# Kernel optimization log

Measured on AMD Instinct MI355X. Metric: run time of the kernel, lower is better.

## Reference

```python
import jax, jax.numpy as jnp
import numpy as np

N_NODES = 50000
N_EDGES = 800000
D_IN = 128
HIDDEN = [128, 128]
D_OUT = 64


def setup_inputs() -> dict:
    key = jax.random.key(0)
    ks = jax.random.split(key, 12)
    x = jax.random.normal(ks[0], (N_NODES, D_IN), dtype=jnp.float32)
    edge_index = jax.random.randint(ks[1], (2, N_EDGES), 0, N_NODES, dtype=jnp.int64)
    # SAGEConv params: lin_l acts on aggregated neighbors (has bias), lin_r on root
    def lin(k, fan_in, fan_out):
        s = 1.0 / np.sqrt(fan_in)
        return jax.random.uniform(k, (fan_in, fan_out), jnp.float32, -s, s)
    dims = [D_IN] + HIDDEN
    inp = {"x": x, "edge_index": edge_index}
    for i in range(len(HIDDEN)):
        inp[f"Wl{i}"] = lin(ks[2 + 3 * i], dims[i], dims[i + 1])
        inp[f"Wr{i}"] = lin(ks[3 + 3 * i], dims[i], dims[i + 1])
        inp[f"b{i}"] = jnp.zeros((dims[i + 1],), jnp.float32)
    inp["Wfc"] = lin(ks[10], HIDDEN[-1], D_OUT)
    inp["bfc"] = jnp.zeros((D_OUT,), jnp.float32)
    return inp


def _sage_conv(x, src, dst, n, Wl, Wr, b, deg_inv):
    # mean-aggregate source features into destination nodes
    agg = jax.ops.segment_sum(x[src], dst, num_segments=n) * deg_inv[:, None]
    return agg @ Wl + x @ Wr + b


def reference(x, edge_index, Wl0, Wr0, b0, Wl1, Wr1, b1, Wfc, bfc):
    src, dst = edge_index[0], edge_index[1]
    n = x.shape[0]
    deg = jax.ops.segment_sum(jnp.ones((src.shape[0],), x.dtype), dst, num_segments=n)
    deg_inv = 1.0 / jnp.maximum(deg, 1.0)
    h = jax.nn.relu(_sage_conv(x, src, dst, n, Wl0, Wr0, b0, deg_inv))
    # dropout p=0 / eval mode -> identity
    h = jax.nn.relu(_sage_conv(h, src, dst, n, Wl1, Wr1, b1, deg_inv))
    return h @ Wfc + bfc
```

## Files before the change

### kernel.cpp

```cpp
#include <hip/hip_runtime.h>
#include <hip/hip_bf16.h>

#define NN 50000
#define NE 800000
#define D 128
#define DOUT 64
#define PAD 64
#define BSH 8
#define NBUCK 196
#define CHUNK 4096
#define NBINB 196
#define SEGC 56
#define N8 (NN * D / 8)

typedef __attribute__((ext_vector_type(8))) short short8;
typedef __attribute__((ext_vector_type(4))) float float4v;


__device__ inline unsigned short f2bf(float f) {
    union { float f; unsigned int i; } c; c.f = f;
    unsigned int u = c.i;
    return (unsigned short)((u + 0x7fffu + ((u >> 16) & 1u)) >> 16);
}
__device__ inline float bflo(unsigned int u) {
    union { unsigned int i; float f; } c; c.i = u << 16; return c.f;
}
__device__ inline float bfhi(unsigned int u) {
    union { unsigned int i; float f; } c; c.i = u & 0xffff0000u; return c.f;
}


struct Stage1Args {
    const int* src;
    const int* dst;
    unsigned int* binned;
    int* cnts;
    const float* W[5];
    unsigned short* P[5];
    const float* x;
    unsigned short* xb;
    unsigned short* zrow;
};

__global__ void stage1(Stage1Args args) {
    int blk = blockIdx.x;
    int tid = threadIdx.x;
    if (blk < NBINB) {
        __shared__ int cnt[NBUCK];
        __shared__ int sh[256];
        __shared__ int lcur[NBUCK];
        __shared__ unsigned int buf[CHUNK];
        int base = blk * CHUNK;
        for (int b = tid; b < NBUCK; b += 256) cnt[b] = 0;
        __syncthreads();
        unsigned int rec[16];
#pragma unroll
        for (int i = 0; i < 16; ++i) {
            int ei = base + i * 256 + tid;
            rec[i] = 0xffffffffu;
            if (ei < NE) {
                unsigned int d = (unsigned int)args.dst[ei];
                unsigned int s = (unsigned int)args.src[ei];
                rec[i] = (d << 16) | s;
                atomicAdd(&cnt[d >> BSH], 1);
            }
        }
        __syncthreads();
        int v = (tid < NBUCK) ? cnt[tid] : 0;
        sh[tid] = v;
        __syncthreads();
        for (int off = 1; off < 256; off <<= 1) {
            int t = (tid >= off) ? sh[tid - off] : 0;
            __syncthreads();
            sh[tid] += t;
            __syncthreads();
        }
        if (tid < NBUCK) {
            lcur[tid] = sh[tid] - cnt[tid];
            args.cnts[blk * NBUCK + tid] = (cnt[tid] < SEGC) ? cnt[tid] : SEGC;
        }
        __syncthreads();
        int total = sh[255];
#pragma unroll
        for (int i = 0; i < 16; ++i) {
            if (rec[i] != 0xffffffffu) {
                int b = rec[i] >> 24;
                int pos = atomicAdd(&lcur[b], 1);
                buf[pos] = rec[i];
            }
        }
        __syncthreads();
        for (int j = tid; j < total; j += 256) {
            unsigned int r = buf[j];
            int q = r >> 24;
            int k = j - (sh[q] - cnt[q]);
            if (k < SEGC)
                args.binned[((size_t)q * NBINB + blk) * SEGC + k] = r;
        }
    } else {
        int b = blk - NBINB;
        if (b < 36) {
            int idx = b * 256 + tid;
            const float* W;
            unsigned short* P;
            int COLS, local;
            if (idx < 4 * 2048) {
                int wsel = idx >> 11;
                W = args.W[wsel]; P = args.P[wsel]; COLS = 128; local = idx & 2047;
            } else {
                W = args.W[4]; P = args.P[4]; COLS = 64; local = idx - 4 * 2048;
            }
            int CT = COLS >> 4;
            int lane = local & 63;
            int fi = local >> 6;
            int ct = fi % CT;
            int kstep = fi / CT;
            int krow = kstep * 32 + (lane >> 4) * 8;
            int col = ct * 16 + (lane & 15);
            unsigned short v[8];
#pragma unroll
            for (int j = 0; j < 8; ++j) v[j] = f2bf(W[(size_t)(krow + j) * COLS + col]);
            unsigned int w0 = v[0] | ((unsigned int)v[1] << 16);
            unsigned int w1 = v[2] | ((unsigned int)v[3] << 16);
            unsigned int w2 = v[4] | ((unsigned int)v[5] << 16);
            unsigned int w3 = v[6] | ((unsigned int)v[7] << 16);
            *(uint4*)(P + (size_t)local * 8) = make_uint4(w0, w1, w2, w3);
            if (b == 0 && tid < 16)
                *(uint4*)(args.zrow + (size_t)tid * 8) = make_uint4(0, 0, 0, 0);
        } else {
            int stride = (gridDim.x - NBINB - 36) * 256;
            for (int i = (b - 36) * 256 + tid; i < N8; i += stride) {
                const float4* p = (const float4*)args.x + (size_t)i * 2;
                float4 a = p[0], bb = p[1];
                unsigned int w0 = f2bf(a.x) | ((unsigned int)f2bf(a.y) << 16);
                unsigned int w1 = f2bf(a.z) | ((unsigned int)f2bf(a.w) << 16);
                unsigned int w2 = f2bf(bb.x) | ((unsigned int)f2bf(bb.y) << 16);
                unsigned int w3 = f2bf(bb.z) | ((unsigned int)f2bf(bb.w) << 16);
                *(uint4*)(args.xb + (size_t)i * 8) = make_uint4(w0, w1, w2, w3);
            }
        }
    }
}


__global__ void scatter_bucket(const unsigned int* __restrict__ binned, const int* __restrict__ cnts,
                               unsigned short* __restrict__ eidx_pad, int* __restrict__ cursor) {
    __shared__ int cur[256];
    __shared__ int segc[NBINB];
    int q = blockIdx.x;
    int tid = threadIdx.x;
    if (tid < 256) cur[tid] = 0;
    for (int s = tid; s < NBINB; s += 512) segc[s] = cnts[(size_t)s * NBUCK + q];
    __syncthreads();
    const unsigned int* bq = binned + (size_t)q * NBINB * SEGC;
    for (int idx = tid; idx < NBINB * SEGC; idx += 512) {
        int seg = idx / SEGC;
        int k = idx - seg * SEGC;
        if (k < segc[seg]) {
            unsigned int r = bq[(size_t)seg * SEGC + k];
            int dl = (r >> 16) & 255;
            int slot = atomicAdd(&cur[dl], 1);
            if (slot < PAD)
                eidx_pad[((size_t)((q << BSH) + dl)) * PAD + slot] = (unsigned short)(r & 0xffffu);
        }
    }
    __syncthreads();
    if (tid < 256) {
        int node = (q << BSH) + tid;
        if (node < NN) cursor[node] = (cur[tid] < PAD) ? cur[tid] : PAD;
    }
}


template <bool FUSEFC>
__global__ __launch_bounds__(256, 4)
void fused_layer(const unsigned short* __restrict__ feat,
                 const int* __restrict__ cursor, const unsigned short* __restrict__ eidx_pad,
                 const unsigned short* __restrict__ zrow,
                 const unsigned short* __restrict__ Pl, const unsigned short* __restrict__ Pr,
                 const float* __restrict__ bias,
                 const unsigned short* __restrict__ Pfc, const float* __restrict__ bfc,
                 unsigned short* __restrict__ outb, float* __restrict__ outf, int n) {
    __shared__ __align__(16) unsigned short As[64][136];

    int tid = threadIdx.x;
    int row0 = blockIdx.x * 64;

    {
        int g = tid >> 4;
        int l = tid & 15;
        int nbase = row0 + g * 4;
        int4 dv = *(const int4*)(cursor + nbase);
        const unsigned short* rbase = eidx_pad + (size_t)nbase * PAD;
        uint4 ia = *(const uint4*)(rbase);
        uint4 ib = *(const uint4*)(rbase + 8);
#pragma unroll
        for (int nn = 0; nn < 4; ++nn) {
            int r = g * 4 + nn;
            int node = nbase + nn;
            uint4 ca = ia, cb = ib;
            if (nn < 3) {
                ia = *(const uint4*)(rbase + (nn + 1) * PAD);
                ib = *(const uint4*)(rbase + (nn + 1) * PAD + 8);
            }
            int deg = 0;
            if (node < n) deg = ((const int*)&dv)[nn];
            float di = 1.0f / (float)(deg > 1 ? deg : 1);
            float acc[8] = {0.f, 0.f, 0.f, 0.f, 0.f, 0.f, 0.f, 0.f};
            {
                int id[16];
                id[0] = ca.x & 0xffff;  id[1] = ca.x >> 16;
                id[2] = ca.y & 0xffff;  id[3] = ca.y >> 16;
                id[4] = ca.z & 0xffff;  id[5] = ca.z >> 16;
                id[6] = ca.w & 0xffff;  id[7] = ca.w >> 16;
                id[8] = cb.x & 0xffff;  id[9] = cb.x >> 16;
                id[10] = cb.y & 0xffff; id[11] = cb.y >> 16;
                id[12] = cb.z & 0xffff; id[13] = cb.z >> 16;
                id[14] = cb.w & 0xffff; id[15] = cb.w >> 16;
                uint4 v[16];
#pragma unroll
                for (int k = 0; k < 16; ++k) {
                    const unsigned short* sp = (k < deg) ? (feat + (size_t)id[k] * D) : zrow;
                    v[k] = *(const uint4*)(sp + l * 8);
                }
#pragma unroll
                for (int k = 0; k < 16; ++k) {
                    acc[0] += bflo(v[k].x); acc[1] += bfhi(v[k].x);
                    acc[2] += bflo(v[k].y); acc[3] += bfhi(v[k].y);
                    acc[4] += bflo(v[k].z); acc[5] += bfhi(v[k].z);
                    acc[6] += bflo(v[k].w); acc[7] += bfhi(v[k].w);
                }
                const unsigned short* rowp = rbase + nn * PAD;
                int p = 16;
                while (p < deg) {
                    uint4 iv = *(const uint4*)(rowp + p);
                    int jd[8];
                    jd[0] = iv.x & 0xffff; jd[1] = iv.x >> 16;
                    jd[2] = iv.y & 0xffff; jd[3] = iv.y >> 16;
                    jd[4] = iv.z & 0xffff; jd[5] = iv.z >> 16;
                    jd[6] = iv.w & 0xffff; jd[7] = iv.w >> 16;
                    uint4 w[8];
#pragma unroll
                    for (int k = 0; k < 8; ++k) {
                        const unsigned short* sp = (p + k < deg) ? (feat + (size_t)jd[k] * D) : zrow;
                        w[k] = *(const uint4*)(sp + l * 8);
                    }
#pragma unroll
                    for (int k = 0; k < 8; ++k) {
                        acc[0] += bflo(w[k].x); acc[1] += bfhi(w[k].x);
                        acc[2] += bflo(w[k].y); acc[3] += bfhi(w[k].y);
                        acc[4] += bflo(w[k].z); acc[5] += bfhi(w[k].z);
                        acc[6] += bflo(w[k].w); acc[7] += bfhi(w[k].w);
                    }
                    p += 8;
                }
            }
            unsigned int w0 = f2bf(acc[0] * di) | ((unsigned int)f2bf(acc[1] * di) << 16);
            unsigned int w1 = f2bf(acc[2] * di) | ((unsigned int)f2bf(acc[3] * di) << 16);
            unsigned int w2 = f2bf(acc[4] * di) | ((unsigned int)f2bf(acc[5] * di) << 16);
            unsigned int w3 = f2bf(acc[6] * di) | ((unsigned int)f2bf(acc[7] * di) << 16);
            *(uint4*)&As[r][l * 8] = make_uint4(w0, w1, w2, w3);
        }
    }

    int wave = tid >> 6;
    int lane = tid & 63;
    int m16 = lane & 15;
    int quad = lane >> 4;
    int rt0 = (wave & 1) * 32;
    int ctb = (wave >> 1) * 4;

    float4v acc[2][4];
#pragma unroll
    for (int t = 0; t < 2; ++t)
#pragma unroll
        for (int c = 0; c < 4; ++c) acc[t][c] = (float4v){0.f, 0.f, 0.f, 0.f};

#pragma unroll
    for (int ks = 0; ks < 4; ++ks) {
        short8 xf[2];
#pragma unroll
        for (int t = 0; t < 2; ++t) {
            int row = row0 + rt0 + t * 16 + m16;
            short8 z = {0, 0, 0, 0, 0, 0, 0, 0};
            xf[t] = (row < n) ? *(const short8*)(feat + (size_t)row * D + ks * 32 + quad * 8) : z;
        }
#pragma unroll
        for (int c = 0; c < 4; ++c) {
            short8 bf = *(const short8*)(Pr + ((size_t)((ks * 8 + ctb + c) * 64 + lane)) * 8);
#pragma unroll
            for (int t = 0; t < 2; ++t)
                acc[t][c] = __builtin_amdgcn_mfma_f32_16x16x32_bf16(xf[t], bf, acc[t][c], 0, 0, 0);
        }
    }

    __syncthreads();

#pragma unroll
    for (int ks = 0; ks < 4; ++ks) {
        short8 af[2];
#pragma unroll
        for (int t = 0; t < 2; ++t)
            af[t] = *(const short8*)&As[rt0 + t * 16 + m16][ks * 32 + quad * 8];
#pragma unroll
        for (int c = 0; c < 4; ++c) {
            short8 bf = *(const short8*)(Pl + ((size_t)((ks * 8 + ctb + c) * 64 + lane)) * 8);
#pragma unroll
            for (int t = 0; t < 2; ++t)
                acc[t][c] = __builtin_amdgcn_mfma_f32_16x16x32_bf16(af[t], bf, acc[t][c], 0, 0, 0);
        }
    }

    if (!FUSEFC) {
#pragma unroll
        for (int t = 0; t < 2; ++t) {
#pragma unroll
            for (int c = 0; c < 4; ++c) {
                int col = (ctb + c) * 16 + m16;
                float bv = bias[col];
#pragma unroll
                for (int i = 0; i < 4; ++i) {
                    int row = row0 + rt0 + t * 16 + quad * 4 + i;
                    if (row < n)
                        outb[(size_t)row * D + col] = f2bf(fmaxf(acc[t][c][i] + bv, 0.f));
                }
            }
        }
    } else {
        __syncthreads();
#pragma unroll
        for (int t = 0; t < 2; ++t) {
#pragma unroll
            for (int c = 0; c < 4; ++c) {
                int col = (ctb + c) * 16 + m16;
                float bv = bias[col];
#pragma unroll
                for (int i = 0; i < 4; ++i) {
                    int row = rt0 + t * 16 + quad * 4 + i;
                    As[row][col] = f2bf(fmaxf(acc[t][c][i] + bv, 0.f));
                }
            }
        }
        __syncthreads();

        int ctbF = (wave >> 1) * 2;
        float4v acc2[2][2];
#pragma unroll
        for (int t = 0; t < 2; ++t)
#pragma unroll
            for (int c = 0; c < 2; ++c) acc2[t][c] = (float4v){0.f, 0.f, 0.f, 0.f};
#pragma unroll
        for (int ks = 0; ks < 4; ++ks) {
            short8 hf[2];
#pragma unroll
            for (int t = 0; t < 2; ++t)
                hf[t] = *(const short8*)&As[rt0 + t * 16 + m16][ks * 32 + quad * 8];
#pragma unroll
            for (int c = 0; c < 2; ++c) {
                short8 bf = *(const short8*)(Pfc + ((size_t)((ks * 4 + ctbF + c) * 64 + lane)) * 8);
#pragma unroll
                for (int t = 0; t < 2; ++t)
                    acc2[t][c] = __builtin_amdgcn_mfma_f32_16x16x32_bf16(hf[t], bf, acc2[t][c], 0, 0, 0);
            }
        }
#pragma unroll
        for (int t = 0; t < 2; ++t) {
#pragma unroll
            for (int c = 0; c < 2; ++c) {
                int col = (ctbF + c) * 16 + m16;
                float bv = bfc[col];
#pragma unroll
                for (int i = 0; i < 4; ++i) {
                    int row = row0 + rt0 + t * 16 + quad * 4 + i;
                    if (row < n)
                        outf[(size_t)row * DOUT + col] = acc2[t][c][i] + bv;
                }
            }
        }
    }
}


extern "C" void kernel_launch(void* const* d_in, const int* in_sizes, int n_in,
                              void* d_out, int out_size, void* d_ws, size_t ws_size,
                              hipStream_t stream) {
    const float* x   = (const float*)d_in[0];
    const int*   ei  = (const int*)d_in[1];
    const float* Wl0 = (const float*)d_in[2];
    const float* Wr0 = (const float*)d_in[3];
    const float* b0  = (const float*)d_in[4];
    const float* Wl1 = (const float*)d_in[5];
    const float* Wr1 = (const float*)d_in[6];
    const float* b1  = (const float*)d_in[7];
    const float* Wfc = (const float*)d_in[8];
    const float* bfc = (const float*)d_in[9];
    float* out = (float*)d_out;

    const int* src = ei;
    const int* dst = ei + NE;

    char* p = (char*)d_ws;
    auto carve = [&](size_t bytes) {
        char* q = p;
        p += (bytes + 255) & ~(size_t)255;
        return q;
    };
    int*            cursor   = (int*)carve(NN * sizeof(int));
    int*            cnts     = (int*)carve((size_t)NBINB * NBUCK * sizeof(int));
    unsigned short* zrow     = (unsigned short*)carve(256);
    unsigned int*   binned   = (unsigned int*)carve((size_t)NBUCK * NBINB * SEGC * 4);
    unsigned short* eidx_pad = (unsigned short*)carve((size_t)NN * PAD * 2);
    unsigned short* xb   = (unsigned short*)carve((size_t)NN * D * 2);
    unsigned short* h0b  = (unsigned short*)carve((size_t)NN * D * 2);
    unsigned short* Wl0p = (unsigned short*)carve(D * D * 2);
    unsigned short* Wr0p = (unsigned short*)carve(D * D * 2);
    unsigned short* Wl1p = (unsigned short*)carve(D * D * 2);
    unsigned short* Wr1p = (unsigned short*)carve(D * D * 2);
    unsigned short* Wfcp = (unsigned short*)carve(D * DOUT * 2);

    Stage1Args sa;
    sa.src = src; sa.dst = dst;
    sa.binned = binned; sa.cnts = cnts;
    sa.W[0] = Wl0; sa.W[1] = Wr0; sa.W[2] = Wl1; sa.W[3] = Wr1; sa.W[4] = Wfc;
    sa.P[0] = Wl0p; sa.P[1] = Wr0p; sa.P[2] = Wl1p; sa.P[3] = Wr1p; sa.P[4] = Wfcp;
    sa.x = x; sa.xb = xb; sa.zrow = zrow;
    stage1<<<NBINB + 256, 256, 0, stream>>>(sa);

    scatter_bucket<<<NBUCK, 512, 0, stream>>>(binned, cnts, eidx_pad, cursor);

    const int GB = (NN + 63) / 64;

    fused_layer<false><<<GB, 256, 0, stream>>>(xb, cursor, eidx_pad, zrow, Wl0p, Wr0p, b0,
                                               nullptr, nullptr, h0b, nullptr, NN);
    fused_layer<true><<<GB, 256, 0, stream>>>(h0b, cursor, eidx_pad, zrow, Wl1p, Wr1p, b1,
                                              Wfcp, bfc, nullptr, out, NN);
}
```

Baseline: 183.6 us.

## Degree-sort nodes within 64-row tiles to balance gather work across thread groups

The scatter kernel now computes, for each 64-node tile, a permutation ordering nodes by descending degree. The fused layer kernels assign nodes to 16-lane groups in a snake pattern over that order, so each group handles a mix of high and low degree nodes. Results are written back to the original LDS rows. The aim is to reduce load imbalance and divergence in the neighbor-gather loop, at the cost of an extra rank computation, a perm buffer, and less contiguous index and cursor loads.

```diff
diff --git a/kernel.cpp b/kernel.cpp
--- a/kernel.cpp
+++ b/kernel.cpp
@@ -2,6 +2,7 @@
 #include <hip/hip_bf16.h>
 
 #define NN 50000
+#define NNP 50176
 #define NE 800000
 #define D 128
 #define DOUT 64
@@ -144,7 +145,8 @@
 
 
 __global__ void scatter_bucket(const unsigned int* __restrict__ binned, const int* __restrict__ cnts,
-                               unsigned short* __restrict__ eidx_pad, int* __restrict__ cursor) {
+                               unsigned short* __restrict__ eidx_pad, int* __restrict__ cursor,
+                               unsigned char* __restrict__ perm) {
     __shared__ int cur[256];
     __shared__ int segc[NBINB];
     int q = blockIdx.x;
@@ -167,7 +169,22 @@
     __syncthreads();
     if (tid < 256) {
         int node = (q << BSH) + tid;
-        if (node < NN) cursor[node] = (cur[tid] < PAD) ? cur[tid] : PAD;
+        int d = (cur[tid] < PAD) ? cur[tid] : PAD;
+        if (node < NN) cursor[node] = d;
+        cur[tid] = d;
+    }
+    __syncthreads();
+    if (tid < 256) {
+        int t = tid >> 6;
+        int i = tid & 63;
+        int d = cur[tid];
+        int rank = 0;
+#pragma unroll 8
+        for (int j = 0; j < 64; ++j) {
+            int dj = cur[(t << 6) | j];
+            rank += (dj > d) || (dj == d && j < i);
+        }
+        perm[(size_t)(q << BSH) + (t << 6) + rank] = (unsigned char)i;
     }
 }
 
@@ -176,6 +193,7 @@
 __global__ __launch_bounds__(256, 4)
 void fused_layer(const unsigned short* __restrict__ feat,
                  const int* __restrict__ cursor, const unsigned short* __restrict__ eidx_pad,
+                 const unsigned char* __restrict__ perm,
                  const unsigned short* __restrict__ zrow,
                  const unsigned short* __restrict__ Pl, const unsigned short* __restrict__ Pr,
                  const float* __restrict__ bias,
@@ -189,22 +207,30 @@
     {
         int g = tid >> 4;
         int l = tid & 15;
-        int nbase = row0 + g * 4;
-        int4 dv = *(const int4*)(cursor + nbase);
-        const unsigned short* rbase = eidx_pad + (size_t)nbase * PAD;
-        uint4 ia = *(const uint4*)(rbase);
-        uint4 ib = *(const uint4*)(rbase + 8);
+        const unsigned char* pm = perm + row0;
+        int li[4], dg[4];
+        li[0] = pm[g];
+        li[1] = pm[31 - g];
+        li[2] = pm[32 + g];
+        li[3] = pm[63 - g];
 #pragma unroll
         for (int nn = 0; nn < 4; ++nn) {
-            int r = g * 4 + nn;
-            int node = nbase + nn;
+            int node = row0 + li[nn];
+            dg[nn] = (node < n) ? cursor[node] : 0;
+        }
+        const unsigned short* rp0 = eidx_pad + (size_t)(row0 + li[0]) * PAD;
+        uint4 ia = *(const uint4*)rp0;
+        uint4 ib = *(const uint4*)(rp0 + 8);
+#pragma unroll
+        for (int nn = 0; nn < 4; ++nn) {
             uint4 ca = ia, cb = ib;
+            const unsigned short* rowp = eidx_pad + (size_t)(row0 + li[nn]) * PAD;
             if (nn < 3) {
-                ia = *(const uint4*)(rbase + (nn + 1) * PAD);
-                ib = *(const uint4*)(rbase + (nn + 1) * PAD + 8);
-            }
-            int deg = 0;
-            if (node < n) deg = ((const int*)&dv)[nn];
+                const unsigned short* rpn = eidx_pad + (size_t)(row0 + li[nn + 1]) * PAD;
+                ia = *(const uint4*)rpn;
+                ib = *(const uint4*)(rpn + 8);
+            }
+            int deg = dg[nn];
             float di = 1.0f / (float)(deg > 1 ? deg : 1);
             float acc[8] = {0.f, 0.f, 0.f, 0.f, 0.f, 0.f, 0.f, 0.f};
             {
@@ -230,7 +256,6 @@
                     acc[4] += bflo(v[k].z); acc[5] += bfhi(v[k].z);
                     acc[6] += bflo(v[k].w); acc[7] += bfhi(v[k].w);
                 }
-                const unsigned short* rowp = rbase + nn * PAD;
                 int p = 16;
                 while (p < deg) {
                     uint4 iv = *(const uint4*)(rowp + p);
@@ -259,7 +284,7 @@
             unsigned int w1 = f2bf(acc[2] * di) | ((unsigned int)f2bf(acc[3] * di) << 16);
             unsigned int w2 = f2bf(acc[4] * di) | ((unsigned int)f2bf(acc[5] * di) << 16);
             unsigned int w3 = f2bf(acc[6] * di) | ((unsigned int)f2bf(acc[7] * di) << 16);
-            *(uint4*)&As[r][l * 8] = make_uint4(w0, w1, w2, w3);
+            *(uint4*)&As[li[nn]][l * 8] = make_uint4(w0, w1, w2, w3);
         }
     }
 
@@ -405,11 +430,12 @@
         p += (bytes + 255) & ~(size_t)255;
         return q;
     };
-    int*            cursor   = (int*)carve(NN * sizeof(int));
+    int*            cursor   = (int*)carve(NNP * sizeof(int));
     int*            cnts     = (int*)carve((size_t)NBINB * NBUCK * sizeof(int));
+    unsigned char*  perm     = (unsigned char*)carve(NNP);
     unsigned short* zrow     = (unsigned short*)carve(256);
     unsigned int*   binned   = (unsigned int*)carve((size_t)NBUCK * NBINB * SEGC * 4);
-    unsigned short* eidx_pad = (unsigned short*)carve((size_t)NN * PAD * 2);
+    unsigned short* eidx_pad = (unsigned short*)carve((size_t)NNP * PAD * 2);
     unsigned short* xb   = (unsigned short*)carve((size_t)NN * D * 2);
     unsigned short* h0b  = (unsigned short*)carve((size_t)NN * D * 2);
     unsigned short* Wl0p = (unsigned short*)carve(D * D * 2);
@@ -426,12 +452,12 @@
     sa.x = x; sa.xb = xb; sa.zrow = zrow;
     stage1<<<NBINB + 256, 256, 0, stream>>>(sa);
 
-    scatter_bucket<<<NBUCK, 512, 0, stream>>>(binned, cnts, eidx_pad, cursor);
+    scatter_bucket<<<NBUCK, 512, 0, stream>>>(binned, cnts, eidx_pad, cursor, perm);
 
     const int GB = (NN + 63) / 64;
 
-    fused_layer<false><<<GB, 256, 0, stream>>>(xb, cursor, eidx_pad, zrow, Wl0p, Wr0p, b0,
+    fused_layer<false><<<GB, 256, 0, stream>>>(xb, cursor, eidx_pad, perm, zrow, Wl0p, Wr0p, b0,
                                                nullptr, nullptr, h0b, nullptr, NN);
-    fused_layer<true><<<GB, 256, 0, stream>>>(h0b, cursor, eidx_pad, zrow, Wl1p, Wr1p, b1,
+    fused_layer<true><<<GB, 256, 0, stream>>>(h0b, cursor, eidx_pad, perm, zrow, Wl1p, Wr1p, b1,
                                               Wfcp, bfc, nullptr, out, NN);
 }
```

Result: no change. 184.6 us (+0.6%).
